# Kernel tuning notes

Hardware: AMD Instinct MI355X
Metric: run time of the kernel (lower is better)

The kernel has to match this reference:

```python
import jax, jax.numpy as jnp
import numpy as np

NUM_HEADS = 8
EMBED_DIM = 512


def _attention(q, k, v, mask=None):
    # q,k,v: [batch, heads, Lq, d] / [batch, heads, Lk, d]
    s = jnp.einsum('bhqd,bhkd->bhqk', q, k)
    if mask is not None:
        s = jnp.where(mask, jnp.asarray(-1000.0, s.dtype), s)
    p = jax.nn.softmax(s, axis=-1)
    return jnp.einsum('bhqk,bhkd->bhqd', p, v)


def _t_mask(T, H):
    # True where attention is DISALLOWED (query frame t_q < key frame t_k)
    tq = jnp.arange(T)[:, None]
    tk = jnp.arange(T)[None, :]
    blocked = tq < tk  # [T, T]
    m = jnp.repeat(jnp.repeat(blocked, H, axis=0), H, axis=1)  # [T*H, T*H]
    return m


def setup_inputs() -> dict:
    key = jax.random.key(0)
    ks = jax.random.split(key, 10)
    B, T, H, W, E = 4, 4, 28, 28, EMBED_DIM
    N = T * H * W
    s_in = (2.0 / (E + 3 * E)) ** 0.5  # xavier-ish
    s_sq = (1.0 / E) ** 0.5
    return {
        'x': jax.random.normal(ks[0], (B, N, E), dtype=jnp.float32),
        'in_proj_weight': jax.random.normal(ks[1], (3 * E, E), dtype=jnp.float32) * s_in,
        'in_proj_bias': jnp.zeros((3 * E,), dtype=jnp.float32),
        'out_proj_w': jax.random.normal(ks[2], (E, E), dtype=jnp.float32) * s_sq,
        'out_proj_b': jnp.zeros((E,), dtype=jnp.float32),
        'in_proj_weight_t': jax.random.normal(ks[3], (E, E), dtype=jnp.float32) * s_sq,
        'in_proj_bias_t': jnp.zeros((E,), dtype=jnp.float32),
        'out_proj_t_w': jax.random.normal(ks[4], (E, E), dtype=jnp.float32) * s_sq,
        'out_proj_t_b': jnp.zeros((E,), dtype=jnp.float32),
        'alpha': 0.0001 * jnp.ones((E,), dtype=jnp.float32),
        'H': 28,
        'W': 28,
    }


def reference(x, in_proj_weight, in_proj_bias, out_proj_w, out_proj_b,
              in_proj_weight_t, in_proj_bias_t, out_proj_t_w, out_proj_t_b,
              alpha, H, W):
    B, N, C = x.shape
    nh = NUM_HEADS
    hc = C // nh
    T = N // (H * W)
    scale = hc ** (-0.5)

    # ---- spatial (per-frame) attention: _forward_2d ----
    qkv = x @ in_proj_weight.T + in_proj_bias            # [B, N, 3C]
    qkv = qkv.reshape(B, T, H * W, 3, nh, hc)
    qkv = qkv.transpose(3, 0, 1, 4, 2, 5).reshape(3, B * T, nh, H * W, hc)
    q, k, v = qkv[0], qkv[1], qkv[2]
    o = _attention(q * scale, k, v)                       # [B*T, nh, HW, hc]
    xs = o.transpose(0, 2, 1, 3).reshape(B, N, C)
    xs = xs @ out_proj_w.T + out_proj_b

    ks = jax.lax.stop_gradient(k)                         # detached cache
    vs = jax.lax.stop_gradient(v)

    # ---- axial temporal attention ----
    q_t = (x @ in_proj_weight_t.T + in_proj_bias_t) * scale  # [B, N, C]
    q_t = q_t.reshape(B, T, H, W, nh, hc)
    q_th = q_t.transpose(0, 3, 4, 1, 2, 5).reshape(B * W, nh, T * H, hc)
    q_tw = q_t.transpose(0, 2, 4, 1, 3, 5).reshape(B * H, nh, T * W, hc)

    k6 = ks.reshape(B, T, nh, H, W, hc)
    v6 = vs.reshape(B, T, nh, H, W, hc)
    k_th = k6.transpose(0, 4, 2, 1, 3, 5).reshape(B * W, nh, T * H, hc)
    k_tw = k6.transpose(0, 3, 2, 1, 4, 5).reshape(B * H, nh, T * W, hc)
    v_th = v6.transpose(0, 4, 2, 1, 3, 5).reshape(B * W, nh, T * H, hc)
    v_tw = v6.transpose(0, 3, 2, 1, 4, 5).reshape(B * H, nh, T * W, hc)

    o_th = _attention(q_th, k_th, v_th, _t_mask(T, H))    # [B*W, nh, T*H, hc]
    o_tw = _attention(q_tw, k_tw, v_tw, _t_mask(T, W))    # [B*H, nh, T*W, hc]

    o_th = o_th.reshape(B, W, nh, T, H, hc).transpose(0, 3, 4, 1, 2, 5).reshape(B, N, C)
    o_tw = o_tw.reshape(B, H, nh, T, W, hc).transpose(0, 3, 1, 4, 2, 5).reshape(B, N, C)

    x_t = (o_th + o_tw) @ out_proj_t_w.T + out_proj_t_b
    return xs + alpha * x_t
```

## Files before the change

### kernel.cpp

```cpp
#include <hip/hip_runtime.h>
#include <stdint.h>

#define NN   3136
#define MM   12544
#define SCALE 0.125f
#define MASKED (-30000.0f)

typedef __attribute__((ext_vector_type(8))) unsigned short ushort8;
typedef __attribute__((ext_vector_type(8))) short short8;
typedef __attribute__((ext_vector_type(4))) float floatx4;

__device__ __forceinline__ float b2f(unsigned short u) {
    union { unsigned int i; float f; } x; x.i = ((unsigned int)u) << 16; return x.f;
}
__device__ __forceinline__ unsigned short f2b(float f) {
    union { float f; unsigned int i; } x; x.f = f;
    unsigned int r = x.i + 0x7fffu + ((x.i >> 16) & 1u);
    return (unsigned short)(r >> 16);
}
__device__ __forceinline__ void load8(const void* p, size_t e, int isf32, float o[8]) {
    if (isf32) {
        const float* f = (const float*)p + e;
        #pragma unroll
        for (int i = 0; i < 8; ++i) o[i] = f[i];
    } else {
        ushort8 u = *(const ushort8*)((const unsigned short*)p + e);
        #pragma unroll
        for (int i = 0; i < 8; ++i) o[i] = b2f(u[i]);
    }
}
__device__ __forceinline__ float load1(const void* p, int e, int isf32) {
    return isf32 ? ((const float*)p)[e] : b2f(((const unsigned short*)p)[e]);
}

__global__ void detect_dtype(const void* __restrict__ x, int* __restrict__ flagp)
{
    if (threadIdx.x == 0 && blockIdx.x == 0) {
        const unsigned short* u = (const unsigned short*)x;
        int c = 0;
        for (int i = 0; i < 512; ++i) {
            const float v = b2f(u[i]);
            if (!(v == v) || fabsf(v) > 1000.0f) ++c;
        }
        *flagp = (c >= 16) ? 1 : 0;
    }
}

__global__ __launch_bounds__(256) void convert_x(
    const int* __restrict__ flagp, const float* __restrict__ x,
    unsigned short* __restrict__ xb)
{
    if (!*flagp) return;
    const size_t i = ((size_t)blockIdx.x * 256 + threadIdx.x) * 8;
    const float4 a = *(const float4*)(x + i);
    const float4 b = *(const float4*)(x + i + 4);
    ushort8 o;
    o[0] = f2b(a.x); o[1] = f2b(a.y); o[2] = f2b(a.z); o[3] = f2b(a.w);
    o[4] = f2b(b.x); o[5] = f2b(b.y); o[6] = f2b(b.z); o[7] = f2b(b.w);
    *(ushort8*)(xb + i) = o;
}

__global__ __launch_bounds__(256) void convert_wp(
    const int* __restrict__ flagp, const void* __restrict__ Wi,
    const void* __restrict__ Wt, unsigned short* __restrict__ wp)
{
    const int isf32 = *flagp;
    const size_t e = ((size_t)blockIdx.x * 256 + threadIdx.x) * 8;
    const int row = (int)(e >> 9);
    const int col = (int)(e & 511);
    float v[8];
    if (row < 1536) load8(Wi, (size_t)row * 512 + col, isf32, v);
    else {
        load8(Wt, (size_t)(row - 1536) * 512 + col, isf32, v);
        #pragma unroll
        for (int u = 0; u < 8; ++u) v[u] *= SCALE;
    }
    ushort8 o;
    #pragma unroll
    for (int u = 0; u < 8; ++u) o[u] = f2b(v[u]);
    *(ushort8*)(wp + e) = o;
}

__global__ __launch_bounds__(256) void convert_wf(
    const int* __restrict__ flagp, const void* __restrict__ Wo,
    const void* __restrict__ Wto, const void* __restrict__ alp,
    unsigned short* __restrict__ qkv)
{
    const int isf32 = *flagp;
    const size_t e = ((size_t)blockIdx.x * 256 + threadIdx.x) * 8;
    const int row = (int)(e >> 10);
    const int k = (int)(e & 1023);
    float v[8];
    if (k < 512) load8(Wo, (size_t)row * 512 + k, isf32, v);
    else {
        const float a = load1(alp, row, isf32);
        load8(Wto, (size_t)row * 512 + (k - 512), isf32, v);
        #pragma unroll
        for (int u = 0; u < 8; ++u) v[u] *= a;
    }
    ushort8 o;
    #pragma unroll
    for (int u = 0; u < 8; ++u) o[u] = f2b(v[u]);
    *(ushort8*)(qkv + (size_t)row * 1536 + 512 + k) = o;
}

__global__ __launch_bounds__(256) void gemm_proj_mfma(
    const int* __restrict__ flagp, const void* __restrict__ x,
    const unsigned short* __restrict__ xb,
    const unsigned short* __restrict__ wp,
    const void* __restrict__ bi, const void* __restrict__ bt,
    unsigned short* __restrict__ qkv, unsigned short* __restrict__ qt)
{
    __shared__ unsigned short A_sh[128][40];
    __shared__ unsigned short B_sh[64][40];
    const int gid = blockIdx.x;
    const int mt = (gid >> 8) * 8 + (gid & 7);
    const int nt = (gid & 255) >> 3;
    if (mt >= 98) return;
    const int m0 = mt * 128, n0 = nt * 64;

    const int isf32 = *flagp;
    const unsigned short* A = isf32 ? xb : (const unsigned short*)x;
    const int tid = threadIdx.x, lane = tid & 63, wv = tid >> 6;
    const int lane15 = lane & 15, quad = lane >> 4;
    const int wm = wv >> 1, wn = wv & 1;

    const int ra = tid >> 1, ca = (tid & 1) * 16;
    const int rb = tid >> 2, cb = (tid & 3) * 8;
    const int nb = n0 + rb;

    floatx4 acc[4][2];
    #pragma unroll
    for (int i = 0; i < 4; ++i)
        #pragma unroll
        for (int j = 0; j < 2; ++j) acc[i][j] = (floatx4){0.f,0.f,0.f,0.f};

    for (int k0 = 0; k0 < 512; k0 += 32) {
        const unsigned short* ap = A + (size_t)(m0 + ra) * 512 + k0 + ca;
        *(ushort8*)&A_sh[ra][ca]     = *(const ushort8*)ap;
        *(ushort8*)&A_sh[ra][ca + 8] = *(const ushort8*)(ap + 8);
        *(ushort8*)&B_sh[rb][cb] = *(const ushort8*)(wp + (size_t)nb * 512 + k0 + cb);
        __syncthreads();

        short8 af[4], bf[2];
        #pragma unroll
        for (int i = 0; i < 4; ++i)
            af[i] = *(const short8*)&A_sh[wm * 64 + i * 16 + lane15][quad * 8];
        #pragma unroll
        for (int j = 0; j < 2; ++j)
            bf[j] = *(const short8*)&B_sh[wn * 32 + j * 16 + lane15][quad * 8];
        #pragma unroll
        for (int i = 0; i < 4; ++i)
            #pragma unroll
            for (int j = 0; j < 2; ++j)
                acc[i][j] = __builtin_amdgcn_mfma_f32_16x16x32_bf16(af[i], bf[j], acc[i][j], 0, 0, 0);
        __syncthreads();
    }

    #pragma unroll
    for (int j = 0; j < 2; ++j) {
        const int col = n0 + wn * 32 + j * 16 + lane15;
        float bias;
        unsigned short* dst;
        int stride;
        if (col < 1536) { bias = load1(bi, col, isf32); dst = qkv; stride = 1536; }
        else { bias = SCALE * load1(bt, col - 1536, isf32); dst = qt; stride = 512; }
        const int cofs = (col < 1536) ? col : (col - 1536);
        #pragma unroll
        for (int i = 0; i < 4; ++i)
            #pragma unroll
            for (int r = 0; r < 4; ++r) {
                const int m = m0 + wm * 64 + i * 16 + quad * 4 + r;
                dst[(size_t)m * stride + cofs] = f2b(acc[i][j][r] + bias);
            }
    }
}

__global__ __launch_bounds__(256) void gemm_final_mfma(
    const int* __restrict__ flagp,
    const unsigned short* __restrict__ qkv, const unsigned short* __restrict__ qt,
    const void* __restrict__ bo, const void* __restrict__ bto,
    const void* __restrict__ alp, void* __restrict__ outp)
{
    __shared__ unsigned short A_sh[128][40];
    __shared__ unsigned short B_sh[64][40];
    const int gid = blockIdx.x;
    const int mt = (gid >> 6) * 8 + (gid & 7);
    const int nt = (gid & 63) >> 3;
    if (mt >= 98) return;
    const int m0 = mt * 128, n0 = nt * 64;

    const int isf32 = *flagp;
    const int tid = threadIdx.x, lane = tid & 63, wv = tid >> 6;
    const int lane15 = lane & 15, quad = lane >> 4;
    const int wm = wv >> 1, wn = wv & 1;

    const int ra = tid >> 1, ca = (tid & 1) * 16;
    const int rb = tid >> 2, cb = (tid & 3) * 8;
    const int nb = n0 + rb;

    floatx4 acc[4][2];
    #pragma unroll
    for (int i = 0; i < 4; ++i)
        #pragma unroll
        for (int j = 0; j < 2; ++j) acc[i][j] = (floatx4){0.f,0.f,0.f,0.f};

    for (int k0 = 0; k0 < 1024; k0 += 32) {
        const int m = m0 + ra;
        const unsigned short* ap = (k0 < 512)
            ? qkv + (size_t)m * 1536 + k0 + ca
            : qt  + (size_t)m * 512  + (k0 - 512) + ca;
        *(ushort8*)&A_sh[ra][ca]     = *(const ushort8*)ap;
        *(ushort8*)&A_sh[ra][ca + 8] = *(const ushort8*)(ap + 8);
        *(ushort8*)&B_sh[rb][cb] =
            *(const ushort8*)(qkv + (size_t)nb * 1536 + 512 + k0 + cb);
        __syncthreads();

        short8 af[4], bf[2];
        #pragma unroll
        for (int i = 0; i < 4; ++i)
            af[i] = *(const short8*)&A_sh[wm * 64 + i * 16 + lane15][quad * 8];
        #pragma unroll
        for (int j = 0; j < 2; ++j)
            bf[j] = *(const short8*)&B_sh[wn * 32 + j * 16 + lane15][quad * 8];
        #pragma unroll
        for (int i = 0; i < 4; ++i)
            #pragma unroll
            for (int j = 0; j < 2; ++j)
                acc[i][j] = __builtin_amdgcn_mfma_f32_16x16x32_bf16(af[i], bf[j], acc[i][j], 0, 0, 0);
        __syncthreads();
    }

    #pragma unroll
    for (int j = 0; j < 2; ++j) {
        const int col = n0 + wn * 32 + j * 16 + lane15;
        const float bias = load1(bo, col, isf32) + load1(alp, col, isf32) * load1(bto, col, isf32);
        #pragma unroll
        for (int i = 0; i < 4; ++i)
            #pragma unroll
            for (int r = 0; r < 4; ++r) {
                const int m = m0 + wm * 64 + i * 16 + quad * 4 + r;
                const float val = acc[i][j][r] + bias;
                const size_t idx = (size_t)m * 512 + col;
                if (isf32) ((float*)outp)[idx] = val;
                else       ((unsigned short*)outp)[idx] = f2b(val);
            }
    }
}

__global__ __launch_bounds__(256) void attn_spatial_mfma(unsigned short* __restrict__ qkv)
{
    __shared__ unsigned short K_sh[64][72];
    __shared__ unsigned short VT_sh[64][72];
    __shared__ unsigned short P_sh[4][16][72];

    const int tid = threadIdx.x, lane = tid & 63, wv = tid >> 6;
    const int lane15 = lane & 15, quad = lane >> 4;

    const int gid = blockIdx.x;
    const int xcd = gid & 7, kk = gid >> 3;
    const int grp = xcd * 16 + kk / 13;
    const int qb  = kk % 13;
    const int head = grp & 7, bt = grp >> 3;

    const int qt_idx = qb * 4 + wv;
    const bool active = (qt_idx < 49);
    const int q0 = active ? qt_idx * 16 : 0;
    const int frame0 = bt * 784;

    short8 q_lo = {0,0,0,0,0,0,0,0}, q_hi = {0,0,0,0,0,0,0,0};
    if (active) {
        const unsigned short* qp = qkv + (size_t)(frame0 + q0 + lane15) * 1536 + head * 64 + quad * 8;
        q_lo = *(const short8*)qp;
        q_hi = *(const short8*)(qp + 32);
    }

    floatx4 accO[4] = {{0.f,0.f,0.f,0.f},{0.f,0.f,0.f,0.f},{0.f,0.f,0.f,0.f},{0.f,0.f,0.f,0.f}};
    float lsum[4] = {0.f, 0.f, 0.f, 0.f};

    const int r_st = tid >> 2, c_st = (tid & 3) << 4;
    const int swzv = c_st;
    const int swzp = (lane15 >> 2) << 4;

    for (int kt = 0; kt < 13; ++kt) {
        __syncthreads();
        ushort8 k8a = {0,0,0,0,0,0,0,0}, k8b = {0,0,0,0,0,0,0,0};
        ushort8 v8a = {0,0,0,0,0,0,0,0}, v8b = {0,0,0,0,0,0,0,0};
        const int key = kt * 64 + r_st;
        if (key < 784) {
            const unsigned short* kp = qkv + (size_t)(frame0 + key) * 1536 + head * 64 + c_st;
            k8a = *(const ushort8*)(kp + 512);
            k8b = *(const ushort8*)(kp + 520);
            v8a = *(const ushort8*)(kp + 1024);
            v8b = *(const ushort8*)(kp + 1032);
        }
        *(ushort8*)&K_sh[r_st][c_st]     = k8a;
        *(ushort8*)&K_sh[r_st][c_st + 8] = k8b;
        #pragma unroll
        for (int u = 0; u < 8; ++u) {
            VT_sh[c_st + u][r_st ^ swzv]     = v8a[u];
            VT_sh[c_st + 8 + u][r_st ^ swzv] = v8b[u];
        }
        __syncthreads();
        if (!active) continue;

        floatx4 s[4];
        #pragma unroll
        for (int st = 0; st < 4; ++st) {
            const short8 kfl = *(const short8*)&K_sh[st * 16 + lane15][quad * 8];
            const short8 kfh = *(const short8*)&K_sh[st * 16 + lane15][32 + quad * 8];
            floatx4 a = {0.f,0.f,0.f,0.f};
            a = __builtin_amdgcn_mfma_f32_16x16x32_bf16(q_lo, kfl, a, 0, 0, 0);
            a = __builtin_amdgcn_mfma_f32_16x16x32_bf16(q_hi, kfh, a, 0, 0, 0);
            s[st] = a;
        }

        const bool tail = (kt == 12);
        #pragma unroll
        for (int st = 0; st < 4; ++st)
            #pragma unroll
            for (int r = 0; r < 4; ++r) {
                const float v = (tail && st >= 1) ? MASKED : s[st][r] * SCALE;
                const float p = __expf(v);
                lsum[r] += p;
                P_sh[wv][quad * 4 + r][(st * 16 + lane15) ^ (quad << 4)] = f2b(p);
            }

        #pragma unroll
        for (int kc = 0; kc < 2; ++kc) {
            const short8 pf = *(const short8*)&P_sh[wv][lane15][(kc * 32 + quad * 8) ^ swzp];
            #pragma unroll
            for (int nt = 0; nt < 4; ++nt) {
                const short8 vf = *(const short8*)&VT_sh[nt * 16 + lane15][(kc * 32 + quad * 8) ^ (nt << 4)];
                accO[nt] = __builtin_amdgcn_mfma_f32_16x16x32_bf16(pf, vf, accO[nt], 0, 0, 0);
            }
        }
    }

    #pragma unroll
    for (int off = 1; off < 16; off <<= 1)
        #pragma unroll
        for (int r = 0; r < 4; ++r)
            lsum[r] += __shfl_xor(lsum[r], off, 64);

    if (active) {
        #pragma unroll
        for (int nt = 0; nt < 4; ++nt)
            #pragma unroll
            for (int r = 0; r < 4; ++r) {
                const int qrow = q0 + quad * 4 + r;
                qkv[(size_t)(frame0 + qrow) * 1536 + head * 64 + nt * 16 + lane15]
                    = f2b(accO[nt][r] / lsum[r]);
            }
    }
}

__global__ __launch_bounds__(256) void attn_axial(
    const unsigned short* __restrict__ qkv, const unsigned short* __restrict__ qtu,
    const unsigned short* __restrict__ oth, unsigned short* __restrict__ outp,
    const int pass)
{
    __shared__ unsigned short K_sh[112][72];
    __shared__ unsigned short VT_sh[64][136];
    __shared__ unsigned short P_sh[4][16][136];

    const int tid = threadIdx.x, lane = tid & 63, wv = tid >> 6;
    const int lane15 = lane & 15, quad = lane >> 4;
    const int b = blockIdx.x / 28, pos = blockIdx.x % 28;
    const int head = blockIdx.y;
    const int r_st = tid >> 3, c_st = (tid & 7) << 3;
    const int swzp = (lane15 >> 2) << 4;

    #pragma unroll
    for (int rnd = 0; rnd < 4; ++rnd) {
        const int j = rnd * 32 + r_st;
        if (j < 112) {
            const int tk = j / 28, rk = j % 28;
            const int n_k = tk * 784 + (pass == 0 ? rk * 28 + pos : pos * 28 + rk);
            const unsigned short* kp = qkv + (size_t)(b * NN + n_k) * 1536 + 512 + head * 64 + c_st;
            const ushort8 k8 = *(const ushort8*)kp;
            const ushort8 v8 = *(const ushort8*)(kp + 512);
            *(ushort8*)&K_sh[j][c_st] = k8;
            #pragma unroll
            for (int u = 0; u < 8; ++u) VT_sh[c_st + u][j ^ c_st] = v8[u];
        } else {
            #pragma unroll
            for (int u = 0; u < 8; ++u) VT_sh[c_st + u][j ^ c_st] = 0;
        }
    }
    __syncthreads();

    for (int tile = wv; tile < 7; tile += 4) {
        const int iq = tile * 16 + lane15;
        const int tq_q = iq / 28, rq = iq % 28;
        const int n_q = tq_q * 784 + (pass == 0 ? rq * 28 + pos : pos * 28 + rq);
        const size_t qaddr = (size_t)(b * NN + n_q) * 512 + head * 64;
        const short8 q_lo = *(const short8*)(qtu + qaddr + quad * 8);
        const short8 q_hi = *(const short8*)(qtu + qaddr + 32 + quad * 8);

        floatx4 s[7];
        #pragma unroll
        for (int st = 0; st < 7; ++st) {
            const short8 kfl = *(const short8*)&K_sh[st * 16 + lane15][quad * 8];
            const short8 kfh = *(const short8*)&K_sh[st * 16 + lane15][32 + quad * 8];
            floatx4 acc = {0.f,0.f,0.f,0.f};
            acc = __builtin_amdgcn_mfma_f32_16x16x32_bf16(q_lo, kfl, acc, 0, 0, 0);
            acc = __builtin_amdgcn_mfma_f32_16x16x32_bf16(q_hi, kfh, acc, 0, 0, 0);
            s[st] = acc;
        }

        int tq_row[4];
        #pragma unroll
        for (int r = 0; r < 4; ++r) tq_row[r] = (tile * 16 + quad * 4 + r) / 28;
        float l[4] = {0.f, 0.f, 0.f, 0.f};
        #pragma unroll
        for (int st = 0; st < 7; ++st) {
            const int tk = (st * 16 + lane15) / 28;
            #pragma unroll
            for (int r = 0; r < 4; ++r) {
                const float v = (tk <= tq_row[r]) ? s[st][r] : MASKED;
                const float p = __expf(v);
                s[st][r] = p;
                l[r] += p;
            }
        }
        #pragma unroll
        for (int off = 1; off < 16; off <<= 1)
            #pragma unroll
            for (int r = 0; r < 4; ++r)
                l[r] += __shfl_xor(l[r], off, 64);

        #pragma unroll
        for (int r = 0; r < 4; ++r) {
            const int row = quad * 4 + r;
            #pragma unroll
            for (int st = 0; st < 7; ++st)
                P_sh[wv][row][(st * 16 + lane15) ^ (quad << 4)] = f2b(s[st][r]);
            P_sh[wv][row][(112 + lane15) ^ (quad << 4)] = 0;
        }

        floatx4 accO[4] = {{0.f,0.f,0.f,0.f},{0.f,0.f,0.f,0.f},{0.f,0.f,0.f,0.f},{0.f,0.f,0.f,0.f}};
        #pragma unroll
        for (int kc = 0; kc < 4; ++kc) {
            const short8 pf = *(const short8*)&P_sh[wv][lane15][(kc * 32 + quad * 8) ^ swzp];
            #pragma unroll
            for (int nt = 0; nt < 4; ++nt) {
                const int row = nt * 16 + lane15;
                const short8 vf = *(const short8*)&VT_sh[row][(kc * 32 + quad * 8) ^ ((row >> 3) << 3)];
                accO[nt] = __builtin_amdgcn_mfma_f32_16x16x32_bf16(pf, vf, accO[nt], 0, 0, 0);
            }
        }

        #pragma unroll
        for (int r = 0; r < 4; ++r) {
            const int io = tile * 16 + quad * 4 + r;
            const int to = io / 28, ro = io % 28;
            const int n_o = to * 784 + (pass == 0 ? ro * 28 + pos : pos * 28 + ro);
            const size_t oaddr = (size_t)(b * NN + n_o) * 512 + head * 64;
            #pragma unroll
            for (int nt = 0; nt < 4; ++nt) {
                float o = accO[nt][r] / l[r];
                if (pass == 1) o += b2f(oth[oaddr + nt * 16 + lane15]);
                outp[oaddr + nt * 16 + lane15] = f2b(o);
            }
        }
    }
}

__global__ void fill_val(unsigned short* o, unsigned short v, int n) {
    const int i = blockIdx.x * 256 + threadIdx.x;
    if (i < n) o[i] = v;
}

extern "C" void kernel_launch(void* const* d_in, const int* in_sizes, int n_in,
                              void* d_out, int out_size, void* d_ws, size_t ws_size,
                              hipStream_t stream)
{
    const void* x   = d_in[0];
    const void* Wi  = d_in[1];
    const void* bi  = d_in[2];
    const void* Wo  = d_in[3];
    const void* bo  = d_in[4];
    const void* Wt  = d_in[5];
    const void* bt  = d_in[6];
    const void* Wto = d_in[7];
    const void* bto = d_in[8];
    const void* alp = d_in[9];

    const size_t QKV_ELEMS = (size_t)MM * 1536;
    const size_t QT_ELEMS  = (size_t)MM * 512;
    const size_t FLAG_OFF  = (QKV_ELEMS + QT_ELEMS) * 2;
    const size_t NEED      = FLAG_OFF + 256;

    if (ws_size < NEED) {
        fill_val<<<dim3((out_size + 255) / 256), dim3(256), 0, stream>>>(
            (unsigned short*)d_out, (unsigned short)0x3f80, out_size);
        return;
    }

    unsigned short* qkv = (unsigned short*)d_ws;
    unsigned short* qt  = qkv + QKV_ELEMS;
    int* flagp = (int*)((char*)d_ws + FLAG_OFF);
    unsigned short* oth = (unsigned short*)d_out;
    unsigned short* xb  = oth + (size_t)MM * 512;
    unsigned short* wp  = oth;

    dim3 blk(256);
    detect_dtype<<<dim3(1), dim3(64), 0, stream>>>(x, flagp);
    convert_x<<<dim3(MM * 512 / (256 * 8)), blk, 0, stream>>>(flagp, (const float*)x, xb);
    convert_wp<<<dim3(2048 * 512 / (256 * 8)), blk, 0, stream>>>(flagp, Wi, Wt, wp);
    gemm_proj_mfma<<<dim3(13 * 256), blk, 0, stream>>>(
        flagp, x, xb, wp, bi, bt, qkv, qt);
    attn_spatial_mfma<<<dim3(13 * 128), blk, 0, stream>>>(qkv);
    attn_axial<<<dim3(112, 8), blk, 0, stream>>>(qkv, qt, nullptr, oth, 0);
    attn_axial<<<dim3(112, 8), blk, 0, stream>>>(qkv, qt, oth, qt, 1);
    convert_wf<<<dim3(512 * 1024 / (256 * 8)), blk, 0, stream>>>(flagp, Wo, Wto, alp, qkv);
    gemm_final_mfma<<<dim3(13 * 64), blk, 0, stream>>>(
        flagp, qkv, qt, bo, bto, alp, d_out);
}
```

Baseline: 305.6 us.

## Fold softmax scale into K weights, use exp2, widen spatial attention blocks

The attention scale times log2(e) is now folded into the K rows of the projection weights and bias. The temporal query projection is no longer scaled, and both attention kernels use the hardware exp2 in place of expf with a per-score multiply. The spatial attention kernel moves to 512-thread blocks of 8 waves, so each K/V tile staged in shared memory serves twice as many query tiles, and the grid shrinks to match. The V-transpose swizzle and the early skip for inactive waves are dropped, which may bring LDS bank conflicts and some wasted MFMA work on the last block.

```diff
diff --git a/kernel.cpp b/kernel.cpp
--- a/kernel.cpp
+++ b/kernel.cpp
@@ -4,6 +4,7 @@
 #define NN   3136
 #define MM   12544
 #define SCALE 0.125f
+#define KSCL  (0.125f * 1.44269504088896f)
 #define MASKED (-30000.0f)
 
 typedef __attribute__((ext_vector_type(8))) unsigned short ushort8;
@@ -17,6 +18,9 @@
     union { float f; unsigned int i; } x; x.f = f;
     unsigned int r = x.i + 0x7fffu + ((x.i >> 16) & 1u);
     return (unsigned short)(r >> 16);
+}
+__device__ __forceinline__ float fexp2(float x) {
+    return __builtin_amdgcn_exp2f(x);
 }
 __device__ __forceinline__ void load8(const void* p, size_t e, int isf32, float o[8]) {
     if (isf32) {
@@ -70,10 +74,10 @@
     const int col = (int)(e & 511);
     float v[8];
     if (row < 1536) load8(Wi, (size_t)row * 512 + col, isf32, v);
-    else {
-        load8(Wt, (size_t)(row - 1536) * 512 + col, isf32, v);
-        #pragma unroll
-        for (int u = 0; u < 8; ++u) v[u] *= SCALE;
+    else            load8(Wt, (size_t)(row - 1536) * 512 + col, isf32, v);
+    if (row >= 512 && row < 1024) {
+        #pragma unroll
+        for (int u = 0; u < 8; ++u) v[u] *= KSCL;
     }
     ushort8 o;
     #pragma unroll
@@ -163,8 +167,12 @@
         float bias;
         unsigned short* dst;
         int stride;
-        if (col < 1536) { bias = load1(bi, col, isf32); dst = qkv; stride = 1536; }
-        else { bias = SCALE * load1(bt, col - 1536, isf32); dst = qt; stride = 512; }
+        if (col < 1536) {
+            bias = load1(bi, col, isf32);
+            if (col >= 512 && col < 1024) bias *= KSCL;
+            dst = qkv; stride = 1536;
+        }
+        else { bias = load1(bt, col - 1536, isf32); dst = qt; stride = 512; }
         const int cofs = (col < 1536) ? col : (col - 1536);
         #pragma unroll
         for (int i = 0; i < 4; ++i)
@@ -248,61 +256,53 @@
     }
 }
 
-__global__ __launch_bounds__(256) void attn_spatial_mfma(unsigned short* __restrict__ qkv)
+__global__ __launch_bounds__(512) void attn_spatial_mfma(unsigned short* __restrict__ qkv)
 {
     __shared__ unsigned short K_sh[64][72];
     __shared__ unsigned short VT_sh[64][72];
-    __shared__ unsigned short P_sh[4][16][72];
+    __shared__ unsigned short P_sh[8][16][72];
 
     const int tid = threadIdx.x, lane = tid & 63, wv = tid >> 6;
     const int lane15 = lane & 15, quad = lane >> 4;
 
     const int gid = blockIdx.x;
     const int xcd = gid & 7, kk = gid >> 3;
-    const int grp = xcd * 16 + kk / 13;
-    const int qb  = kk % 13;
+    const int grp = xcd * 16 + kk / 7;
+    const int qb  = kk % 7;
     const int head = grp & 7, bt = grp >> 3;
 
-    const int qt_idx = qb * 4 + wv;
-    const bool active = (qt_idx < 49);
-    const int q0 = active ? qt_idx * 16 : 0;
+    const int t0 = qb * 8 + wv;
+    const bool act = (t0 < 49);
+    const int q0 = act ? t0 * 16 : 0;
     const int frame0 = bt * 784;
 
     short8 q_lo = {0,0,0,0,0,0,0,0}, q_hi = {0,0,0,0,0,0,0,0};
-    if (active) {
+    if (act) {
         const unsigned short* qp = qkv + (size_t)(frame0 + q0 + lane15) * 1536 + head * 64 + quad * 8;
         q_lo = *(const short8*)qp;
         q_hi = *(const short8*)(qp + 32);
     }
 
     floatx4 accO[4] = {{0.f,0.f,0.f,0.f},{0.f,0.f,0.f,0.f},{0.f,0.f,0.f,0.f},{0.f,0.f,0.f,0.f}};
-    float lsum[4] = {0.f, 0.f, 0.f, 0.f};
-
-    const int r_st = tid >> 2, c_st = (tid & 3) << 4;
-    const int swzv = c_st;
-    const int swzp = (lane15 >> 2) << 4;
+    float ls[4] = {0.f, 0.f, 0.f, 0.f};
+
+    const int key_l = tid & 63;
+    const int cs    = (tid >> 6) * 8;
+    const int swzp  = (lane15 >> 2) << 4;
 
     for (int kt = 0; kt < 13; ++kt) {
         __syncthreads();
-        ushort8 k8a = {0,0,0,0,0,0,0,0}, k8b = {0,0,0,0,0,0,0,0};
-        ushort8 v8a = {0,0,0,0,0,0,0,0}, v8b = {0,0,0,0,0,0,0,0};
-        const int key = kt * 64 + r_st;
+        const int key = kt * 64 + key_l;
+        ushort8 k8 = {0,0,0,0,0,0,0,0}, v8 = {0,0,0,0,0,0,0,0};
         if (key < 784) {
-            const unsigned short* kp = qkv + (size_t)(frame0 + key) * 1536 + head * 64 + c_st;
-            k8a = *(const ushort8*)(kp + 512);
-            k8b = *(const ushort8*)(kp + 520);
-            v8a = *(const ushort8*)(kp + 1024);
-            v8b = *(const ushort8*)(kp + 1032);
-        }
-        *(ushort8*)&K_sh[r_st][c_st]     = k8a;
-        *(ushort8*)&K_sh[r_st][c_st + 8] = k8b;
-        #pragma unroll
-        for (int u = 0; u < 8; ++u) {
-            VT_sh[c_st + u][r_st ^ swzv]     = v8a[u];
-            VT_sh[c_st + 8 + u][r_st ^ swzv] = v8b[u];
-        }
+            const unsigned short* kp = qkv + (size_t)(frame0 + key) * 1536 + head * 64 + cs;
+            k8 = *(const ushort8*)(kp + 512);
+            v8 = *(const ushort8*)(kp + 1024);
+        }
+        *(ushort8*)&K_sh[key_l][cs] = k8;
+        #pragma unroll
+        for (int u = 0; u < 8; ++u) VT_sh[cs + u][key_l] = v8[u];
         __syncthreads();
-        if (!active) continue;
 
         floatx4 s[4];
         #pragma unroll
@@ -320,9 +320,9 @@
         for (int st = 0; st < 4; ++st)
             #pragma unroll
             for (int r = 0; r < 4; ++r) {
-                const float v = (tail && st >= 1) ? MASKED : s[st][r] * SCALE;
-                const float p = __expf(v);
-                lsum[r] += p;
+                const float v = (tail && st >= 1) ? MASKED : s[st][r];
+                const float p = fexp2(v);
+                ls[r] += p;
                 P_sh[wv][quad * 4 + r][(st * 16 + lane15) ^ (quad << 4)] = f2b(p);
             }
 
@@ -331,7 +331,7 @@
             const short8 pf = *(const short8*)&P_sh[wv][lane15][(kc * 32 + quad * 8) ^ swzp];
             #pragma unroll
             for (int nt = 0; nt < 4; ++nt) {
-                const short8 vf = *(const short8*)&VT_sh[nt * 16 + lane15][(kc * 32 + quad * 8) ^ (nt << 4)];
+                const short8 vf = *(const short8*)&VT_sh[nt * 16 + lane15][kc * 32 + quad * 8];
                 accO[nt] = __builtin_amdgcn_mfma_f32_16x16x32_bf16(pf, vf, accO[nt], 0, 0, 0);
             }
         }
@@ -341,16 +341,16 @@
     for (int off = 1; off < 16; off <<= 1)
         #pragma unroll
         for (int r = 0; r < 4; ++r)
-            lsum[r] += __shfl_xor(lsum[r], off, 64);
-
-    if (active) {
+            ls[r] += __shfl_xor(ls[r], off, 64);
+
+    if (act) {
         #pragma unroll
         for (int nt = 0; nt < 4; ++nt)
             #pragma unroll
             for (int r = 0; r < 4; ++r) {
                 const int qrow = q0 + quad * 4 + r;
                 qkv[(size_t)(frame0 + qrow) * 1536 + head * 64 + nt * 16 + lane15]
-                    = f2b(accO[nt][r] / lsum[r]);
+                    = f2b(accO[nt][r] / ls[r]);
             }
     }
 }
@@ -419,7 +419,7 @@
             #pragma unroll
             for (int r = 0; r < 4; ++r) {
                 const float v = (tk <= tq_row[r]) ? s[st][r] : MASKED;
-                const float p = __expf(v);
+                const float p = fexp2(v);
                 s[st][r] = p;
                 l[r] += p;
             }
@@ -511,7 +511,7 @@
     convert_wp<<<dim3(2048 * 512 / (256 * 8)), blk, 0, stream>>>(flagp, Wi, Wt, wp);
     gemm_proj_mfma<<<dim3(13 * 256), blk, 0, stream>>>(
         flagp, x, xb, wp, bi, bt, qkv, qt);
-    attn_spatial_mfma<<<dim3(13 * 128), blk, 0, stream>>>(qkv);
+    attn_spatial_mfma<<<dim3(112 * 8), dim3(512), 0, stream>>>(qkv);
     attn_axial<<<dim3(112, 8), blk, 0, stream>>>(qkv, qt, nullptr, oth, 0);
     attn_axial<<<dim3(112, 8), blk, 0, stream>>>(qkv, qt, oth, qt, 1);
     convert_wf<<<dim3(512 * 1024 / (256 * 8)), blk, 0, stream>>>(flagp, Wo, Wto, alp, qkv);
```

New measurement: 308.3 us. Within noise of the previous version (+0.9%).
